# Kernel tuning notes

Measured on AMD Instinct MI355X. Metric: run time of the kernel, lower is better.

The kernel has to match this reference:

```python
import jax, jax.numpy as jnp
import numpy as np

N_NODES = 100000
N_EDGES = 300000
D = 256
EPS = 1e-5
ALPHA = 0.5  # residual_alpha


def setup_inputs() -> dict:
    key = jax.random.key(0)
    ks = jax.random.split(key, 6)
    x = jax.random.normal(ks[0], (N_NODES, D), dtype=jnp.float32)
    edge_index = jax.random.randint(ks[1], (2, N_EDGES), 0, N_NODES, dtype=jnp.int32)
    edge_weight = jax.random.uniform(ks[2], (N_EDGES,), dtype=jnp.float32)
    # GCNConv parameters (glorot-ish weight, bias)
    W = jax.random.normal(ks[3], (D, D), dtype=jnp.float32) / np.float32(np.sqrt(D))
    b = 0.01 * jax.random.normal(ks[4], (D,), dtype=jnp.float32)
    # LayerNorm parameters
    gamma = jnp.ones((D,), dtype=jnp.float32)
    beta = jnp.zeros((D,), dtype=jnp.float32)
    return {"x": x, "edge_index": edge_index, "edge_weight": edge_weight,
            "W": W, "b": b, "gamma": gamma, "beta": beta}


def gcn_residual(x, edge_index, edge_weight, W, b, gamma, beta):
    src, dst = edge_index[0], edge_index[1]
    # linear transform first (PyG GCNConv order)
    h = x @ W  # [N, D]
    # gcn_norm with added self-loops (self-loop weight = 1)
    deg = jax.ops.segment_sum(edge_weight, dst, num_segments=N_NODES) + 1.0  # [N]
    dinv = jax.lax.rsqrt(deg)
    norm = dinv[src] * edge_weight * dinv[dst]  # [E]
    # message + aggregate (scatter-add over destination nodes)
    agg = jax.ops.segment_sum(norm[:, None] * h[src], dst, num_segments=N_NODES)
    agg = agg + (dinv * dinv)[:, None] * h  # self-loop contribution
    h = agg + b
    # LayerNorm over feature dim
    mu = jnp.mean(h, axis=-1, keepdims=True)
    var = jnp.mean(jnp.square(h - mu), axis=-1, keepdims=True)
    h = (h - mu) * jax.lax.rsqrt(var + EPS) * gamma + beta
    # dropout p=0.0 -> identity; weighted residual; relu
    h = ALPHA * h + (1.0 - ALPHA) * x
    return jax.nn.relu(h)


def reference(x, edge_index, edge_weight, W, b, gamma, beta):
    return gcn_residual(x, edge_index, edge_weight, W, b, gamma, beta)
```

## Files before the change

kernel.cpp:

```cpp
#include <hip/hip_runtime.h>


#define NN 100000
#define NE 300000
#define DD 256
#define NB 391
#define GMB 1563

typedef __attribute__((ext_vector_type(8))) short short8;
typedef __attribute__((ext_vector_type(4))) float f32x4;
typedef __attribute__((ext_vector_type(4))) unsigned short u16x4;

static __device__ __forceinline__ short f2bf(float f) {
  union { float f; unsigned u; } a; a.f = f;
  unsigned r = a.u + 0x7fffu + ((a.u >> 16) & 1u);
  return (short)(r >> 16);
}

static __device__ __forceinline__ float bf2f(short s) {
  return __uint_as_float((unsigned)(unsigned short)s << 16);
}

__global__ __launch_bounds__(256) void k_init(float* __restrict__ dv,
                                              int* __restrict__ cnt) {
  int i = blockIdx.x * 256 + threadIdx.x;
  if (i < NN) { dv[i] = 0.0f; cnt[i] = 0; }
}

__global__ __launch_bounds__(256) void k_hist(const int* __restrict__ ei,
                                              const float* __restrict__ ew,
                                              float* __restrict__ dv,
                                              int* __restrict__ cnt) {
  int e = blockIdx.x * 256 + threadIdx.x;
  if (e < NE) {
    int d = ei[NE + e];
    atomicAdd(&dv[d], ew[e]);
    atomicAdd(&cnt[d], 1);
  }
}

__global__ __launch_bounds__(256) void k_dinv(float* __restrict__ dv) {
  int i = blockIdx.x * 256 + threadIdx.x;
  if (i < NN) dv[i] = rsqrtf(dv[i] + 1.0f);
}

__global__ __launch_bounds__(256) void k_scan1(const int* __restrict__ cnt,
                                               int* __restrict__ off,
                                               int* __restrict__ bsum) {
  __shared__ int tmp[256];
  int t = threadIdx.x;
  int i = blockIdx.x * 256 + t;
  int v = (i < NN) ? cnt[i] : 0;
  tmp[t] = v;
  __syncthreads();
  for (int o = 1; o < 256; o <<= 1) {
    int u = (t >= o) ? tmp[t - o] : 0;
    __syncthreads();
    tmp[t] += u;
    __syncthreads();
  }
  if (i < NN) off[i] = tmp[t] - v;
  if (t == 255) bsum[blockIdx.x] = tmp[t];
}

__global__ __launch_bounds__(512) void k_scan2(int* __restrict__ bsum) {
  __shared__ int tmp[512];
  int t = threadIdx.x;
  int v = (t < NB) ? bsum[t] : 0;
  tmp[t] = v;
  __syncthreads();
  for (int o = 1; o < 512; o <<= 1) {
    int u = (t >= o) ? tmp[t - o] : 0;
    __syncthreads();
    tmp[t] += u;
    __syncthreads();
  }
  bsum[t] = tmp[t] - v;
}

__global__ __launch_bounds__(256) void k_scan3(int* __restrict__ off,
                                               const int* __restrict__ bsum,
                                               int* __restrict__ cur) {
  int i = blockIdx.x * 256 + threadIdx.x;
  if (i < NN) {
    int o = off[i] + bsum[i >> 8];
    off[i] = o;
    cur[i] = o;
  }
}

__global__ __launch_bounds__(256) void k_place(const int* __restrict__ ei,
                                               const float* __restrict__ ew,
                                               const float* __restrict__ dv,
                                               int* __restrict__ cur,
                                               int2* __restrict__ elist) {
  int e = blockIdx.x * 256 + threadIdx.x;
  if (e >= NE) return;
  int s = ei[e];
  int d = ei[NE + e];
  float c = dv[s] * ew[e] * dv[d];
  int pos = atomicAdd(&cur[d], 1);
  elist[pos] = make_int2(s, __float_as_int(c));
}

__global__ __launch_bounds__(256) void k_wprep(const float* __restrict__ W,
                                               short* __restrict__ Wf) {
  int idx = blockIdx.x * 256 + threadIdx.x;
  int k = idx >> 6;
  int c4 = idx & 63;
  const float4 v = *(const float4*)(W + k * 256 + c4 * 4);
  float vv[4] = {v.x, v.y, v.z, v.w};
#pragma unroll
  for (int i = 0; i < 4; ++i) {
    int c = c4 * 4 + i;
    int di = ((k >> 5) * 16 + (c >> 4)) * 512 + ((c & 15) + ((k >> 3) & 3) * 16) * 8 + (k & 7);
    Wf[di] = f2bf(vv[i]);
  }
}

__global__ __launch_bounds__(512, 2) void k_gemm(const float* __restrict__ x,
                                                 const short* __restrict__ Wf,
                                                 short* __restrict__ h) {
  __shared__ short As[64 * 256];

  const int t = threadIdx.x;
  const int lane = t & 63;
  const int wid = t >> 6;
  const int row0 = blockIdx.x * 64;
  const int wrow = (wid >> 2) * 32;
  const int wstrip = wid & 3;

  const int rr = t >> 3;
  const int kc = t & 7;
  int grow = row0 + rr;
  if (grow > NN - 1) grow = NN - 1;
  const float* rp = x + (size_t)grow * 256 + kc * 8;
  float4 a0 = *(const float4*)(rp);        float4 b0 = *(const float4*)(rp + 4);
  float4 a1 = *(const float4*)(rp + 64);   float4 b1 = *(const float4*)(rp + 68);
  float4 a2 = *(const float4*)(rp + 128);  float4 b2 = *(const float4*)(rp + 132);
  float4 a3 = *(const float4*)(rp + 192);  float4 b3 = *(const float4*)(rp + 196);

  const int wb = (rr * 512 + kc * 16) ^ ((rr & 7) << 4);

#define WRITE_REGION(I, A, B)                                              \
  {                                                                        \
    short8 s_;                                                             \
    s_[0] = f2bf(A.x); s_[1] = f2bf(A.y); s_[2] = f2bf(A.z);               \
    s_[3] = f2bf(A.w); s_[4] = f2bf(B.x); s_[5] = f2bf(B.y);               \
    s_[6] = f2bf(B.z); s_[7] = f2bf(B.w);                                  \
    *(short8*)((char*)As + wb + (I)*128) = s_;                             \
  }

#define BARSYNC                                                            \
  asm volatile("s_waitcnt lgkmcnt(0)" ::: "memory");                       \
  __builtin_amdgcn_s_barrier();

  f32x4 acc[4][2];
#pragma unroll
  for (int mc = 0; mc < 4; ++mc)
#pragma unroll
    for (int nr = 0; nr < 2; ++nr) acc[mc][nr] = (f32x4)0.0f;

  const short* wbase = Wf + (size_t)(wstrip * 4) * 512 + lane * 8;

#define COMPUTE_REGION(I)                                                  \
  _Pragma("unroll")                                                        \
  for (int ks2 = 0; ks2 < 2; ++ks2) {                                      \
    const int ks = 2 * (I) + ks2;                                          \
    short8 bx[2];                                                          \
    short8 aw[4];                                                          \
    _Pragma("unroll")                                                      \
    for (int nr = 0; nr < 2; ++nr) {                                       \
      int r_ = wrow + nr * 16 + (lane & 15);                               \
      int byte_ = (r_ * 512 + ks * 64 + (lane >> 4) * 16) ^ ((r_ & 7) << 4); \
      bx[nr] = *(short8*)((char*)As + byte_);                              \
    }                                                                      \
    _Pragma("unroll")                                                      \
    for (int mc = 0; mc < 4; ++mc)                                         \
      aw[mc] = *(const short8*)(wbase + (size_t)(ks * 16 + mc) * 512);     \
    _Pragma("unroll")                                                      \
    for (int mc = 0; mc < 4; ++mc)                                         \
      _Pragma("unroll")                                                    \
      for (int nr = 0; nr < 2; ++nr)                                       \
        acc[mc][nr] = __builtin_amdgcn_mfma_f32_16x16x32_bf16(             \
            aw[mc], bx[nr], acc[mc][nr], 0, 0, 0);                         \
  }

  WRITE_REGION(0, a0, b0);
  BARSYNC;
  COMPUTE_REGION(0);
  WRITE_REGION(1, a1, b1);
  BARSYNC;
  COMPUTE_REGION(1);
  WRITE_REGION(2, a2, b2);
  BARSYNC;
  COMPUTE_REGION(2);
  WRITE_REGION(3, a3, b3);
  BARSYNC;
  COMPUTE_REGION(3);

#undef WRITE_REGION
#undef BARSYNC
#undef COMPUTE_REGION

#pragma unroll
  for (int mc = 0; mc < 4; ++mc) {
    int cbase = wstrip * 64 + mc * 16 + 4 * (lane >> 4);
#pragma unroll
    for (int nr = 0; nr < 2; ++nr) {
      int r = row0 + wrow + nr * 16 + (lane & 15);
      if (r < NN) {
        u16x4 s;
        s[0] = (unsigned short)f2bf(acc[mc][nr][0]);
        s[1] = (unsigned short)f2bf(acc[mc][nr][1]);
        s[2] = (unsigned short)f2bf(acc[mc][nr][2]);
        s[3] = (unsigned short)f2bf(acc[mc][nr][3]);
        *(u16x4*)(h + (size_t)r * 256 + cbase) = s;
      }
    }
  }
}

__global__ __launch_bounds__(256) void k_agg(const short* __restrict__ h,
                                             const float* __restrict__ dv,
                                             const int* __restrict__ cnt,
                                             const int* __restrict__ off,
                                             const int2* __restrict__ elist,
                                             const float* __restrict__ x,
                                             const float* __restrict__ b,
                                             const float* __restrict__ gamma,
                                             const float* __restrict__ beta,
                                             float* __restrict__ out) {
  int node = (blockIdx.x * 256 + threadIdx.x) >> 5;
  if (node >= NN) return;
  int q = threadIdx.x & 31;

  const float di = dv[node];
  const float d2 = di * di;
  short8 hv = *(const short8*)(h + (size_t)node * 256 + q * 8);
  float a[8];
#pragma unroll
  for (int i = 0; i < 8; ++i) a[i] = bf2f(hv[i]) * d2;

  const int n = cnt[node];
  const int st = off[node];
  int j = 0;
  for (; j + 4 <= n; j += 4) {
    int2 r0 = elist[st + j];
    int2 r1 = elist[st + j + 1];
    int2 r2 = elist[st + j + 2];
    int2 r3 = elist[st + j + 3];
    short8 g0 = *(const short8*)(h + (size_t)r0.x * 256 + q * 8);
    short8 g1 = *(const short8*)(h + (size_t)r1.x * 256 + q * 8);
    short8 g2 = *(const short8*)(h + (size_t)r2.x * 256 + q * 8);
    short8 g3 = *(const short8*)(h + (size_t)r3.x * 256 + q * 8);
    float c0 = __int_as_float(r0.y);
    float c1 = __int_as_float(r1.y);
    float c2 = __int_as_float(r2.y);
    float c3 = __int_as_float(r3.y);
#pragma unroll
    for (int i = 0; i < 8; ++i)
      a[i] += c0 * bf2f(g0[i]) + c1 * bf2f(g1[i]) + c2 * bf2f(g2[i]) + c3 * bf2f(g3[i]);
  }
  for (; j < n; ++j) {
    int2 r0 = elist[st + j];
    short8 g0 = *(const short8*)(h + (size_t)r0.x * 256 + q * 8);
    float c0 = __int_as_float(r0.y);
#pragma unroll
    for (int i = 0; i < 8; ++i) a[i] += c0 * bf2f(g0[i]);
  }

  const float4 b0 = *(const float4*)(b + q * 8);
  const float4 b1 = *(const float4*)(b + q * 8 + 4);
  a[0] += b0.x; a[1] += b0.y; a[2] += b0.z; a[3] += b0.w;
  a[4] += b1.x; a[5] += b1.y; a[6] += b1.z; a[7] += b1.w;

  float s = 0.f, ss = 0.f;
#pragma unroll
  for (int i = 0; i < 8; ++i) { s += a[i]; ss += a[i] * a[i]; }
#pragma unroll
  for (int o = 16; o > 0; o >>= 1) {
    s += __shfl_xor(s, o);
    ss += __shfl_xor(ss, o);
  }
  const float mu = s * (1.0f / 256.0f);
  const float var = ss * (1.0f / 256.0f) - mu * mu;
  const float inv = rsqrtf(var + 1e-5f);

  const float4 g0 = *(const float4*)(gamma + q * 8);
  const float4 g1 = *(const float4*)(gamma + q * 8 + 4);
  const float4 e0 = *(const float4*)(beta + q * 8);
  const float4 e1 = *(const float4*)(beta + q * 8 + 4);
  const float4 x0 = *(const float4*)(x + (size_t)node * 256 + q * 8);
  const float4 x1 = *(const float4*)(x + (size_t)node * 256 + q * 8 + 4);

  float4 r0, r1;
  r0.x = fmaxf(0.5f * ((a[0] - mu) * inv * g0.x + e0.x) + 0.5f * x0.x, 0.f);
  r0.y = fmaxf(0.5f * ((a[1] - mu) * inv * g0.y + e0.y) + 0.5f * x0.y, 0.f);
  r0.z = fmaxf(0.5f * ((a[2] - mu) * inv * g0.z + e0.z) + 0.5f * x0.z, 0.f);
  r0.w = fmaxf(0.5f * ((a[3] - mu) * inv * g0.w + e0.w) + 0.5f * x0.w, 0.f);
  r1.x = fmaxf(0.5f * ((a[4] - mu) * inv * g1.x + e1.x) + 0.5f * x1.x, 0.f);
  r1.y = fmaxf(0.5f * ((a[5] - mu) * inv * g1.y + e1.y) + 0.5f * x1.y, 0.f);
  r1.z = fmaxf(0.5f * ((a[6] - mu) * inv * g1.z + e1.z) + 0.5f * x1.z, 0.f);
  r1.w = fmaxf(0.5f * ((a[7] - mu) * inv * g1.w + e1.w) + 0.5f * x1.w, 0.f);

  float* o = out + (size_t)node * 256 + q * 8;
  *(float4*)(o) = r0;
  *(float4*)(o + 4) = r1;
}

extern "C" void kernel_launch(void* const* d_in, const int* in_sizes, int n_in,
                              void* d_out, int out_size, void* d_ws, size_t ws_size,
                              hipStream_t stream) {
  const float* x     = (const float*)d_in[0];
  const int*   ei    = (const int*)d_in[1];
  const float* ew    = (const float*)d_in[2];
  const float* W     = (const float*)d_in[3];
  const float* b     = (const float*)d_in[4];
  const float* gamma = (const float*)d_in[5];
  const float* beta  = (const float*)d_in[6];
  float* out = (float*)d_out;

  short* h   = (short*)d_ws;
  float* dv  = (float*)(h + (size_t)NN * DD);
  int*   cnt = (int*)(dv + NN);
  int*   off = cnt + NN;
  int*   cur = off + NN;
  int*   bsum = cur + NN;
  int2*  elist = (int2*)(bsum + 512);
  short* Wf  = (short*)(elist + NE);

  k_init<<<NB, 256, 0, stream>>>(dv, cnt);
  k_hist<<<(NE + 255) / 256, 256, 0, stream>>>(ei, ew, dv, cnt);
  k_dinv<<<NB, 256, 0, stream>>>(dv);
  k_scan1<<<NB, 256, 0, stream>>>(cnt, off, bsum);
  k_scan2<<<1, 512, 0, stream>>>(bsum);
  k_scan3<<<NB, 256, 0, stream>>>(off, bsum, cur);
  k_place<<<(NE + 255) / 256, 256, 0, stream>>>(ei, ew, dv, cur, elist);

  k_wprep<<<64, 256, 0, stream>>>(W, Wf);
  k_gemm<<<GMB, 512, 0, stream>>>(x, Wf, h);

  k_agg<<<(NN * 32 + 255) / 256, 256, 0, stream>>>(h, dv, cnt, off, elist, x, b, gamma, beta, out);
}
```

Baseline: 164.8 us.

## Fuse dinv into scan, use memset, packed bf16 cvt, branchless gather loop

Several small changes at once. The degree-inverse computation moves into k_scan3, which removes one launch, and k_init is replaced by hipMemsetAsync calls. The GEMM output now uses the hardware v_cvt_pk_bf16_f32 instruction instead of manual rounding, and empty asm barriers pin the loaded x values in registers. The aggregation loop handles tail edges by clamping indices and zeroing their coefficients, which removes the scalar remainder loop at the cost of redundant gathers. The GEMM is also launched before the graph preprocessing.

```diff
diff --git a/kernel.cpp b/kernel.cpp
--- a/kernel.cpp
+++ b/kernel.cpp
@@ -21,10 +21,10 @@
   return __uint_as_float((unsigned)(unsigned short)s << 16);
 }
 
-__global__ __launch_bounds__(256) void k_init(float* __restrict__ dv,
-                                              int* __restrict__ cnt) {
-  int i = blockIdx.x * 256 + threadIdx.x;
-  if (i < NN) { dv[i] = 0.0f; cnt[i] = 0; }
+static __device__ __forceinline__ unsigned cvtpk(float a, float b) {
+  unsigned r;
+  asm("v_cvt_pk_bf16_f32 %0, %1, %2" : "=v"(r) : "v"(a), "v"(b));
+  return r;
 }
 
 __global__ __launch_bounds__(256) void k_hist(const int* __restrict__ ei,
@@ -37,11 +37,6 @@
     atomicAdd(&dv[d], ew[e]);
     atomicAdd(&cnt[d], 1);
   }
-}
-
-__global__ __launch_bounds__(256) void k_dinv(float* __restrict__ dv) {
-  int i = blockIdx.x * 256 + threadIdx.x;
-  if (i < NN) dv[i] = rsqrtf(dv[i] + 1.0f);
 }
 
 __global__ __launch_bounds__(256) void k_scan1(const int* __restrict__ cnt,
@@ -80,12 +75,14 @@
 
 __global__ __launch_bounds__(256) void k_scan3(int* __restrict__ off,
                                                const int* __restrict__ bsum,
-                                               int* __restrict__ cur) {
+                                               int* __restrict__ cur,
+                                               float* __restrict__ dv) {
   int i = blockIdx.x * 256 + threadIdx.x;
   if (i < NN) {
     int o = off[i] + bsum[i >> 8];
     off[i] = o;
     cur[i] = o;
+    dv[i] = rsqrtf(dv[i] + 1.0f);
   }
 }
 
@@ -139,6 +136,15 @@
   float4 a1 = *(const float4*)(rp + 64);   float4 b1 = *(const float4*)(rp + 68);
   float4 a2 = *(const float4*)(rp + 128);  float4 b2 = *(const float4*)(rp + 132);
   float4 a3 = *(const float4*)(rp + 192);  float4 b3 = *(const float4*)(rp + 196);
+
+  asm volatile("" : "+v"(a0.x), "+v"(a0.y), "+v"(a0.z), "+v"(a0.w),
+                    "+v"(b0.x), "+v"(b0.y), "+v"(b0.z), "+v"(b0.w),
+                    "+v"(a1.x), "+v"(a1.y), "+v"(a1.z), "+v"(a1.w),
+                    "+v"(b1.x), "+v"(b1.y), "+v"(b1.z), "+v"(b1.w));
+  asm volatile("" : "+v"(a2.x), "+v"(a2.y), "+v"(a2.z), "+v"(a2.w),
+                    "+v"(b2.x), "+v"(b2.y), "+v"(b2.z), "+v"(b2.w),
+                    "+v"(a3.x), "+v"(a3.y), "+v"(a3.z), "+v"(a3.w),
+                    "+v"(b3.x), "+v"(b3.y), "+v"(b3.z), "+v"(b3.w));
 
   const int wb = (rr * 512 + kc * 16) ^ ((rr & 7) << 4);
 
@@ -210,12 +216,10 @@
     for (int nr = 0; nr < 2; ++nr) {
       int r = row0 + wrow + nr * 16 + (lane & 15);
       if (r < NN) {
-        u16x4 s;
-        s[0] = (unsigned short)f2bf(acc[mc][nr][0]);
-        s[1] = (unsigned short)f2bf(acc[mc][nr][1]);
-        s[2] = (unsigned short)f2bf(acc[mc][nr][2]);
-        s[3] = (unsigned short)f2bf(acc[mc][nr][3]);
-        *(u16x4*)(h + (size_t)r * 256 + cbase) = s;
+        union { u16x4 s; unsigned u[2]; } S;
+        S.u[0] = cvtpk(acc[mc][nr][0], acc[mc][nr][1]);
+        S.u[1] = cvtpk(acc[mc][nr][2], acc[mc][nr][3]);
+        *(u16x4*)(h + (size_t)r * 256 + cbase) = S.s;
       }
     }
   }
@@ -244,30 +248,29 @@
 
   const int n = cnt[node];
   const int st = off[node];
-  int j = 0;
-  for (; j + 4 <= n; j += 4) {
-    int2 r0 = elist[st + j];
-    int2 r1 = elist[st + j + 1];
-    int2 r2 = elist[st + j + 2];
-    int2 r3 = elist[st + j + 3];
-    short8 g0 = *(const short8*)(h + (size_t)r0.x * 256 + q * 8);
-    short8 g1 = *(const short8*)(h + (size_t)r1.x * 256 + q * 8);
-    short8 g2 = *(const short8*)(h + (size_t)r2.x * 256 + q * 8);
-    short8 g3 = *(const short8*)(h + (size_t)r3.x * 256 + q * 8);
-    float c0 = __int_as_float(r0.y);
-    float c1 = __int_as_float(r1.y);
-    float c2 = __int_as_float(r2.y);
-    float c3 = __int_as_float(r3.y);
-#pragma unroll
-    for (int i = 0; i < 8; ++i)
-      a[i] += c0 * bf2f(g0[i]) + c1 * bf2f(g1[i]) + c2 * bf2f(g2[i]) + c3 * bf2f(g3[i]);
-  }
-  for (; j < n; ++j) {
-    int2 r0 = elist[st + j];
-    short8 g0 = *(const short8*)(h + (size_t)r0.x * 256 + q * 8);
-    float c0 = __int_as_float(r0.y);
-#pragma unroll
-    for (int i = 0; i < 8; ++i) a[i] += c0 * bf2f(g0[i]);
+  if (n > 0) {
+    int j = 0;
+    do {
+      const int i1 = (j + 1 < n) ? j + 1 : j;
+      const int i2 = (j + 2 < n) ? j + 2 : j;
+      const int i3 = (j + 3 < n) ? j + 3 : j;
+      int2 r0 = elist[st + j];
+      int2 r1 = elist[st + i1];
+      int2 r2 = elist[st + i2];
+      int2 r3 = elist[st + i3];
+      short8 g0 = *(const short8*)(h + (size_t)r0.x * 256 + q * 8);
+      short8 g1 = *(const short8*)(h + (size_t)r1.x * 256 + q * 8);
+      short8 g2 = *(const short8*)(h + (size_t)r2.x * 256 + q * 8);
+      short8 g3 = *(const short8*)(h + (size_t)r3.x * 256 + q * 8);
+      float c0 = __int_as_float(r0.y);
+      float c1 = (j + 1 < n) ? __int_as_float(r1.y) : 0.f;
+      float c2 = (j + 2 < n) ? __int_as_float(r2.y) : 0.f;
+      float c3 = (j + 3 < n) ? __int_as_float(r3.y) : 0.f;
+#pragma unroll
+      for (int i = 0; i < 8; ++i)
+        a[i] += c0 * bf2f(g0[i]) + c1 * bf2f(g1[i]) + c2 * bf2f(g2[i]) + c3 * bf2f(g3[i]);
+      j += 4;
+    } while (j < n);
   }
 
   const float4 b0 = *(const float4*)(b + q * 8);
@@ -330,16 +333,17 @@
   int2*  elist = (int2*)(bsum + 512);
   short* Wf  = (short*)(elist + NE);
 
-  k_init<<<NB, 256, 0, stream>>>(dv, cnt);
+  (void)hipMemsetAsync(dv, 0, NN * sizeof(float), stream);
+  (void)hipMemsetAsync(cnt, 0, NN * sizeof(int), stream);
+
+  k_wprep<<<64, 256, 0, stream>>>(W, Wf);
+  k_gemm<<<GMB, 512, 0, stream>>>(x, Wf, h);
+
   k_hist<<<(NE + 255) / 256, 256, 0, stream>>>(ei, ew, dv, cnt);
-  k_dinv<<<NB, 256, 0, stream>>>(dv);
   k_scan1<<<NB, 256, 0, stream>>>(cnt, off, bsum);
   k_scan2<<<1, 512, 0, stream>>>(bsum);
-  k_scan3<<<NB, 256, 0, stream>>>(off, bsum, cur);
+  k_scan3<<<NB, 256, 0, stream>>>(off, bsum, cur, dv);
   k_place<<<(NE + 255) / 256, 256, 0, stream>>>(ei, ew, dv, cur, elist);
 
-  k_wprep<<<64, 256, 0, stream>>>(W, Wf);
-  k_gemm<<<GMB, 512, 0, stream>>>(x, Wf, h);
-
   k_agg<<<(NN * 32 + 255) / 256, 256, 0, stream>>>(h, dv, cnt, off, elist, x, b, gamma, beta, out);
 }
```

Result: slower. 170.2 us (+3.3%).
